# Kernel optimization log

Measured on AMD Instinct MI355X. Metric: run time of the kernel, lower is better.

## Reference

```python
import jax, jax.numpy as jnp
import numpy as np

NUM_SIN = 8
HIDDEN = 64
COND = 128
OUT = 4
SQRT2 = 1.4142135623730951


def coords_to_sinusoidals(coords):
    # coords: [..., 2]; per-frequency blocks of 4: [sin_x, sin_y, cos_x, cos_y]
    freqs = 2.0 ** jnp.arange(NUM_SIN, dtype=coords.dtype)  # mult freq_type, multiplier=2
    ang = coords[..., None, :] * freqs[:, None]              # [..., 8, 2]
    emb = jnp.concatenate([jnp.sin(ang), jnp.cos(ang)], axis=-1)  # [..., 8, 4]
    return emb.reshape(coords.shape[:-1] + (2 * 2 * NUM_SIN,))


def equal_linear(x, w, b, lrelu):
    scale = 1.0 / np.sqrt(w.shape[1])  # lr_mul = 1
    y = x @ (w * scale).T + b
    if lrelu:
        y = jax.nn.leaky_relu(y, 0.2) * SQRT2  # fused_lrelu
    return y


def setup_inputs() -> dict:
    key = jax.random.key(0)
    ks = jax.random.split(key, 8)
    coords = jax.random.normal(ks[0], (8, 256, 256, 2), dtype=jnp.float32)
    c = jax.random.normal(ks[1], (8, COND), dtype=jnp.float32)
    freq_unlock = jax.random.uniform(ks[2], (1,), dtype=jnp.float32)
    in1 = 2 * 2 * NUM_SIN + COND  # 160
    in2 = HIDDEN + COND           # 192
    w1 = jax.random.normal(ks[3], (HIDDEN, in1), dtype=jnp.float32)
    w2 = jax.random.normal(ks[4], (HIDDEN, in2), dtype=jnp.float32)
    w3 = jax.random.normal(ks[5], (HIDDEN, in2), dtype=jnp.float32)
    w4 = jax.random.normal(ks[6], (OUT, in2), dtype=jnp.float32)
    b1 = jnp.zeros((HIDDEN,), jnp.float32)
    b2 = jnp.zeros((HIDDEN,), jnp.float32)
    b3 = jnp.zeros((HIDDEN,), jnp.float32)
    b4 = jnp.zeros((OUT,), jnp.float32)
    return {"coords": coords, "c": c, "freq_unlock": freq_unlock,
            "w1": w1, "b1": b1, "w2": w2, "b2": b2,
            "w3": w3, "b3": b3, "w4": w4, "b4": b4}


def reference(coords, c, freq_unlock, w1, b1, w2, b2, w3, b3, w4, b4):
    B, H, W, _ = coords.shape
    emb = coords_to_sinusoidals(coords / 10.0)  # [B,H,W,32]
    # progressive frequency masking
    limits = jnp.arange(1, NUM_SIN + 1, dtype=coords.dtype) / (NUM_SIN + 1)
    weights = jnp.clip((freq_unlock[0] - limits) * (NUM_SIN + 1), 0.0, 1.0)  # [8]
    emb = emb * jnp.repeat(weights, 4)  # blocks of 4 per frequency
    x = emb.reshape(B * H * W, -1)
    cf = jnp.broadcast_to(c[:, None, None, :], (B, H, W, COND)).reshape(B * H * W, COND)
    h = equal_linear(jnp.concatenate([x, cf], -1), w1, b1, True)
    h = equal_linear(jnp.concatenate([h, cf], -1), w2, b2, True)
    h = equal_linear(jnp.concatenate([h, cf], -1), w3, b3, True)
    h = equal_linear(jnp.concatenate([h, cf], -1), w4, b4, False)
    out = h.reshape(B, H, W, OUT)
    # radius masking
    radius = jnp.sqrt(jnp.sum(coords ** 2, axis=-1, keepdims=True))
    out = out * (1.0 - jnp.tanh(jax.nn.relu(radius - 1.0)))
    return out
```

## Files before the change

kernel.cpp:

```cpp
#include <hip/hip_runtime.h>
#include <math.h>


typedef _Float16 half2v __attribute__((ext_vector_type(2)));
typedef __fp16   fp16x2 __attribute__((ext_vector_type(2)));
typedef _Float16 half4v __attribute__((ext_vector_type(4)));
typedef _Float16 half8  __attribute__((ext_vector_type(8)));
typedef float f32x16 __attribute__((ext_vector_type(16)));

#define SCALE1 0.0790569415042094833f
#define SCALE2 0.0721687836487032206f
#define SQRT2F 1.41421356237309515f

#define FE_L1 0
#define FE_L2 256
#define FE_L3 768
#define FE_L4 1280
#define FE_TOT 1536
#define OFF_CB1 6144
#define OFF_CB2 6656
#define OFF_CB3 7168
#define OFF_CB4 7680

__global__ __launch_bounds__(256) void prep_kernel(
    const float* __restrict__ c, const float* __restrict__ fu,
    const float* __restrict__ w1, const float* __restrict__ b1,
    const float* __restrict__ w2, const float* __restrict__ b2,
    const float* __restrict__ w3, const float* __restrict__ b3,
    const float* __restrict__ w4, const float* __restrict__ b4,
    float* __restrict__ ws)
{
  int t = blockIdx.x * 256 + threadIdx.x;
  if (t < 12288) {
    _Float16* fr = (_Float16*)ws;
    int e, Ktm;
    const float* w; float scale; int stride; bool perm;
    if (t < 2048)       { e = t;         Ktm = 2; w = w1; scale = SCALE1;          stride = 160; perm = false; }
    else if (t < 6144)  { e = t - 2048;  Ktm = 4; w = w2; scale = SCALE2 * SQRT2F; stride = 192; perm = true;  }
    else if (t < 10240) { e = t - 6144;  Ktm = 4; w = w3; scale = SCALE2 * SQRT2F; stride = 192; perm = true;  }
    else                { e = t - 10240; Ktm = 4; w = w4; scale = SCALE2 * SQRT2F; stride = 192; perm = true;  }
    int til  = e >> 9;
    int lane = (e >> 3) & 63;
    int r    = e & 7;
    int q    = lane >> 5;
    int mt = til / Ktm, kt = til - mt * Ktm;
    int j = 32 * mt + (lane & 31);
    int k;
    if (perm) {
      k = 32 * (kt >> 1) + 16 * (kt & 1) + 8 * (r >> 2) + 4 * q + (r & 3);
    } else {
      k = 16 * kt + 8 * q + r;
    }
    float val;
    if (t < 2048) {
      float mw = (fu[0] - (float)((k >> 2) + 1) * (1.0f / 9.0f)) * 9.0f;
      mw = fminf(fmaxf(mw, 0.0f), 1.0f);
      val = w[j * stride + k] * scale * mw;
    } else if (t >= 10240) {
      val = (j < 4) ? w[j * stride + k] * scale : 0.0f;
    } else {
      val = w[j * stride + k] * scale;
    }
    fr[t] = (_Float16)val;
  } else {
    int u = t - 12288;
    if (u >= 6272) return;
    int d = u >> 2, part = u & 3;
    const float* wr; float bias; float scale; int outoff;
    int b, j;
    if (d < 1536) {
      int grp = d >> 9;
      b = (d & 511) >> 6; j = d & 63;
      if (grp == 0)      { wr = w1 + j * 160 + 32; bias = b1[j]; scale = SCALE1; outoff = OFF_CB1 + b * 64 + j; }
      else if (grp == 1) { wr = w2 + j * 192 + 64; bias = b2[j]; scale = SCALE2; outoff = OFF_CB2 + b * 64 + j; }
      else               { wr = w3 + j * 192 + 64; bias = b3[j]; scale = SCALE2; outoff = OFF_CB3 + b * 64 + j; }
    } else {
      int u2 = d - 1536;
      b = u2 >> 2; j = u2 & 3;
      wr = w4 + j * 192 + 64; bias = b4[j]; scale = SCALE2; outoff = OFF_CB4 + b * 4 + j;
    }
    const float4* wv = (const float4*)wr + part * 8;
    const float4* cv = (const float4*)(c + b * 128) + part * 8;
    float4 s = make_float4(0.f, 0.f, 0.f, 0.f);
    #pragma unroll
    for (int k = 0; k < 8; ++k) {
      float4 a = wv[k], dd = cv[k];
      s.x = fmaf(a.x, dd.x, s.x);
      s.y = fmaf(a.y, dd.y, s.y);
      s.z = fmaf(a.z, dd.z, s.z);
      s.w = fmaf(a.w, dd.w, s.w);
    }
    float v = (s.x + s.y) + (s.z + s.w);
    v += __shfl_xor(v, 1);
    v += __shfl_xor(v, 2);
    if (part == 0) ws[outoff] = fmaf(scale, v, bias);
  }
}

#define WAIT_VM3() asm volatile("s_waitcnt vmcnt(3)" ::: "memory")
#define WAIT_VM0() asm volatile("s_waitcnt vmcnt(0)" ::: "memory")

__global__ __launch_bounds__(256, 4) void decoder_main(
    const float2* __restrict__ coords, const float* __restrict__ ws,
    float4* __restrict__ out)
{
  __shared__ __align__(16) _Float16 sfr_raw[FE_TOT * 8];
  __shared__ __align__(16) float scb[256];
  half8* __restrict__ sfr = (half8*)sfr_raw;

  const int tid  = threadIdx.x;
  const int lane = tid & 63;
  const int wave = tid >> 6;
  const int b    = blockIdx.x >> 7;
  const int col  = lane & 31;
  const bool hi  = lane >= 32;
  const int q4   = hi ? 4 : 0;

  const float2* __restrict__ cptr = coords + blockIdx.x * 512 + wave * 64;
  float2 cc[2][2];
  cc[0][0] = cptr[col];       cc[0][1] = cptr[32 + col];
  cc[1][0] = cptr[256 + col]; cc[1][1] = cptr[288 + col];
  __builtin_amdgcn_sched_barrier(0);

  if (wave == 3) {
    __builtin_amdgcn_global_load_lds(
        (const __attribute__((address_space(1))) void*)(ws + OFF_CB1 + b * 64 + lane),
        (__attribute__((address_space(3))) void*)(scb + 0), 4, 0, 0);
    __builtin_amdgcn_global_load_lds(
        (const __attribute__((address_space(1))) void*)(ws + OFF_CB2 + b * 64 + lane),
        (__attribute__((address_space(3))) void*)(scb + 64), 4, 0, 0);
    __builtin_amdgcn_global_load_lds(
        (const __attribute__((address_space(1))) void*)(ws + OFF_CB3 + b * 64 + lane),
        (__attribute__((address_space(3))) void*)(scb + 128), 4, 0, 0);
    __builtin_amdgcn_global_load_lds(
        (const __attribute__((address_space(1))) void*)(ws + OFF_CB4 + b * 4 + lane),
        (__attribute__((address_space(3))) void*)(scb + 192), 4, 0, 0);
  }
  __builtin_amdgcn_sched_barrier(0);

  const half8* __restrict__ gfr = (const half8*)ws;
  #pragma unroll
  for (int i = 0; i < 3; ++i) {
    const int e0 = wave * 64 + 256 * i;
    __builtin_amdgcn_global_load_lds(
        (const __attribute__((address_space(1))) void*)(gfr + e0 + lane),
        (__attribute__((address_space(3))) void*)(sfr_raw + e0 * 8),
        16, 0, 0);
  }
  __builtin_amdgcn_sched_barrier(0);
  #pragma unroll
  for (int i = 3; i < 6; ++i) {
    const int e0 = wave * 64 + 256 * i;
    __builtin_amdgcn_global_load_lds(
        (const __attribute__((address_space(1))) void*)(gfr + e0 + lane),
        (__attribute__((address_space(3))) void*)(sfr_raw + e0 * 8),
        16, 0, 0);
  }
  __builtin_amdgcn_sched_barrier(0);

  f32x16 acc[2][2];
  half8 nbf[2][4];

  auto transition = [&]() {
    #pragma unroll
    for (int mt = 0; mt < 2; ++mt)
      #pragma unroll
      for (int nt = 0; nt < 2; ++nt) {
        #pragma unroll
        for (int h = 0; h < 2; ++h) {
          half2v pp[4];
          #pragma unroll
          for (int p = 0; p < 4; ++p) {
            fp16x2 t = __builtin_amdgcn_cvt_pkrtz(acc[mt][nt][8 * h + 2 * p],
                                                  acc[mt][nt][8 * h + 2 * p + 1]);
            pp[p] = __builtin_bit_cast(half2v, t);
          }
          half4v q0 = __builtin_shufflevector(pp[0], pp[1], 0, 1, 2, 3);
          half4v q1 = __builtin_shufflevector(pp[2], pp[3], 0, 1, 2, 3);
          half8 f = __builtin_shufflevector(q0, q1, 0, 1, 2, 3, 4, 5, 6, 7);
          half8 f2 = f * (_Float16)0.2f;
          nbf[nt][2 * mt + h] = __builtin_elementwise_max(f, f2);
        }
      }
  };

  auto init_acc = [&](const float* __restrict__ cb) {
    #pragma unroll
    for (int mt = 0; mt < 2; ++mt)
      #pragma unroll
      for (int g = 0; g < 4; ++g) {
        const float4 f = *(const float4*)(cb + 32 * mt + 8 * g + q4);
        #pragma unroll
        for (int nt = 0; nt < 2; ++nt) {
          acc[mt][nt][4 * g + 0] = f.x;
          acc[mt][nt][4 * g + 1] = f.y;
          acc[mt][nt][4 * g + 2] = f.z;
          acc[mt][nt][4 * g + 3] = f.w;
        }
      }
  };

  #pragma unroll
  for (int t = 0; t < 2; ++t) {
    half8 bf[2][2];
    {
      const float qm = hi ? 0.4f : 0.1f;
      auto chain = [](float a, float* s, float* c) {
        float s0 = __sinf(a), c0 = __cosf(a);
        s[0] = s0; c[0] = c0;
        float s1 = 2.f * s0 * c0, c1 = (c0 - s0) * (c0 + s0);
        s[1] = s1; c[1] = c1;
        float s2 = 2.f * s1 * c1, c2 = (c1 - s1) * (c1 + s1);
        float s3 = 2.f * s2 * c2, c3 = (c2 - s2) * (c2 + s2);
        float s4 = 2.f * s3 * c3, c4 = (c3 - s3) * (c3 + s3);
        s[2] = s4; c[2] = c4;
        float s5 = 2.f * s4 * c4, c5 = (c4 - s4) * (c4 + s4);
        s[3] = s5; c[3] = c5;
      };
      #pragma unroll
      for (int nt = 0; nt < 2; ++nt) {
        const float2 ccv = cc[t][nt];
        float sx[4], cx[4], sy[4], cy[4];
        chain(ccv.x * qm, sx, cx);
        chain(ccv.y * qm, sy, cy);
        #pragma unroll
        for (int kt = 0; kt < 2; ++kt) {
          const int i0 = 2 * kt, i1 = 2 * kt + 1;
          half2v p0v = __builtin_bit_cast(half2v, __builtin_amdgcn_cvt_pkrtz(sx[i0], sy[i0]));
          half2v p1v = __builtin_bit_cast(half2v, __builtin_amdgcn_cvt_pkrtz(cx[i0], cy[i0]));
          half2v p2v = __builtin_bit_cast(half2v, __builtin_amdgcn_cvt_pkrtz(sx[i1], sy[i1]));
          half2v p3v = __builtin_bit_cast(half2v, __builtin_amdgcn_cvt_pkrtz(cx[i1], cy[i1]));
          half4v q0 = __builtin_shufflevector(p0v, p1v, 0, 1, 2, 3);
          half4v q1 = __builtin_shufflevector(p2v, p3v, 0, 1, 2, 3);
          bf[nt][kt] = __builtin_shufflevector(q0, q1, 0, 1, 2, 3, 4, 5, 6, 7);
        }
      }
    }

    if (t == 0) {
      WAIT_VM3();
      __builtin_amdgcn_s_barrier();
      __builtin_amdgcn_sched_barrier(0);
    }

    init_acc(scb + 0);
    #pragma unroll
    for (int kt = 0; kt < 2; ++kt) {
      half8 a0 = sfr[FE_L1 + (0 * 2 + kt) * 64 + lane];
      half8 a1 = sfr[FE_L1 + (1 * 2 + kt) * 64 + lane];
      acc[0][0] = __builtin_amdgcn_mfma_f32_32x32x16_f16(a0, bf[0][kt], acc[0][0], 0, 0, 0);
      acc[0][1] = __builtin_amdgcn_mfma_f32_32x32x16_f16(a0, bf[1][kt], acc[0][1], 0, 0, 0);
      acc[1][0] = __builtin_amdgcn_mfma_f32_32x32x16_f16(a1, bf[0][kt], acc[1][0], 0, 0, 0);
      acc[1][1] = __builtin_amdgcn_mfma_f32_32x32x16_f16(a1, bf[1][kt], acc[1][1], 0, 0, 0);
    }
    transition();

    init_acc(scb + 64);
    #pragma unroll
    for (int kt = 0; kt < 4; ++kt) {
      half8 a0 = sfr[FE_L2 + (0 * 4 + kt) * 64 + lane];
      half8 a1 = sfr[FE_L2 + (1 * 4 + kt) * 64 + lane];
      acc[0][0] = __builtin_amdgcn_mfma_f32_32x32x16_f16(a0, nbf[0][kt], acc[0][0], 0, 0, 0);
      acc[0][1] = __builtin_amdgcn_mfma_f32_32x32x16_f16(a0, nbf[1][kt], acc[0][1], 0, 0, 0);
      acc[1][0] = __builtin_amdgcn_mfma_f32_32x32x16_f16(a1, nbf[0][kt], acc[1][0], 0, 0, 0);
      acc[1][1] = __builtin_amdgcn_mfma_f32_32x32x16_f16(a1, nbf[1][kt], acc[1][1], 0, 0, 0);
    }
    transition();

    if (t == 0) {
      WAIT_VM0();
      __builtin_amdgcn_s_barrier();
      __builtin_amdgcn_sched_barrier(0);
    }

    init_acc(scb + 128);
    #pragma unroll
    for (int kt = 0; kt < 4; ++kt) {
      half8 a0 = sfr[FE_L3 + (0 * 4 + kt) * 64 + lane];
      half8 a1 = sfr[FE_L3 + (1 * 4 + kt) * 64 + lane];
      acc[0][0] = __builtin_amdgcn_mfma_f32_32x32x16_f16(a0, nbf[0][kt], acc[0][0], 0, 0, 0);
      acc[0][1] = __builtin_amdgcn_mfma_f32_32x32x16_f16(a0, nbf[1][kt], acc[0][1], 0, 0, 0);
      acc[1][0] = __builtin_amdgcn_mfma_f32_32x32x16_f16(a1, nbf[0][kt], acc[1][0], 0, 0, 0);
      acc[1][1] = __builtin_amdgcn_mfma_f32_32x32x16_f16(a1, nbf[1][kt], acc[1][1], 0, 0, 0);
    }
    transition();

    f32x16 acc4[2];
    {
      const float c0 = scb[192], c1 = scb[193], c2 = scb[194], c3 = scb[195];
      #pragma unroll
      for (int r = 0; r < 16; ++r) { acc4[0][r] = 0.f; acc4[1][r] = 0.f; }
      if (!hi) {
        acc4[0][0] = c0; acc4[0][1] = c1; acc4[0][2] = c2; acc4[0][3] = c3;
        acc4[1][0] = c0; acc4[1][1] = c1; acc4[1][2] = c2; acc4[1][3] = c3;
      }
    }
    #pragma unroll
    for (int kt = 0; kt < 4; ++kt) {
      half8 a0 = sfr[FE_L4 + kt * 64 + lane];
      acc4[0] = __builtin_amdgcn_mfma_f32_32x32x16_f16(a0, nbf[0][kt], acc4[0], 0, 0, 0);
      acc4[1] = __builtin_amdgcn_mfma_f32_32x32x16_f16(a0, nbf[1][kt], acc4[1], 0, 0, 0);
    }

    if (!hi) {
      const int pbase = blockIdx.x * 512 + t * 256 + wave * 64 + col;
      #pragma unroll
      for (int nt = 0; nt < 2; ++nt) {
        const float2 ccv = cc[t][nt];
        const float rad = sqrtf(ccv.x * ccv.x + ccv.y * ccv.y);
        const float tt = fmaxf(rad - 1.0f, 0.0f);
        const float m = 2.0f / (__expf(2.0f * tt) + 1.0f);
        out[pbase + 32 * nt] = make_float4(acc4[nt][0] * m, acc4[nt][1] * m,
                                           acc4[nt][2] * m, acc4[nt][3] * m);
      }
    }
  }
}

extern "C" void kernel_launch(void* const* d_in, const int* in_sizes, int n_in,
                              void* d_out, int out_size, void* d_ws, size_t ws_size,
                              hipStream_t stream) {
  const float* coords = (const float*)d_in[0];
  const float* c      = (const float*)d_in[1];
  const float* fu     = (const float*)d_in[2];
  const float* w1     = (const float*)d_in[3];
  const float* b1     = (const float*)d_in[4];
  const float* w2     = (const float*)d_in[5];
  const float* b2     = (const float*)d_in[6];
  const float* w3     = (const float*)d_in[7];
  const float* b3     = (const float*)d_in[8];
  const float* w4     = (const float*)d_in[9];
  const float* b4     = (const float*)d_in[10];
  float* ws  = (float*)d_ws;
  float* out = (float*)d_out;

  int npix = in_sizes[0] / 2;

  prep_kernel<<<73, 256, 0, stream>>>(c, fu, w1, b1, w2, b2, w3, b3, w4, b4, ws);
  decoder_main<<<npix / 512, 256, 0, stream>>>(
      (const float2*)coords, ws, (float4*)out);
}
```

Measured before the change: 92.70 us.

## Initialize accumulators via bias MFMA with split-fp16 bias fragments

The per-image conditioning bias is now written by the prep kernel as fp16 hi/lo pairs laid out as MFMA A-fragments, alongside the weights. The main kernel loads them into LDS with the weight fragments and produces each layer's initial accumulator with an MFMA against a ones vector, instead of filling 16-wide accumulators from LDS float4 reads and register moves. The radius mask computation is hoisted earlier so it overlaps other work. This trades VALU/LDS accumulator initialization for extra MFMA issues and a larger LDS footprint, which could lower occupancy.

```diff
diff --git a/kernel.cpp b/kernel.cpp
--- a/kernel.cpp
+++ b/kernel.cpp
@@ -17,10 +17,8 @@
 #define FE_L3 768
 #define FE_L4 1280
 #define FE_TOT 1536
-#define OFF_CB1 6144
-#define OFF_CB2 6656
-#define OFF_CB3 7168
-#define OFF_CB4 7680
+#define BE_BASE 1536
+#define BIAS_PER_IMG 512
 
 __global__ __launch_bounds__(256) void prep_kernel(
     const float* __restrict__ c, const float* __restrict__ fu,
@@ -62,22 +60,23 @@
       val = w[j * stride + k] * scale;
     }
     fr[t] = (_Float16)val;
-  } else {
+  } else if (t < 18560) {
     int u = t - 12288;
-    if (u >= 6272) return;
     int d = u >> 2, part = u & 3;
-    const float* wr; float bias; float scale; int outoff;
-    int b, j;
+    const float* wr; float bias; float scale;
+    int b, j, entry, lidx;
     if (d < 1536) {
       int grp = d >> 9;
       b = (d & 511) >> 6; j = d & 63;
-      if (grp == 0)      { wr = w1 + j * 160 + 32; bias = b1[j]; scale = SCALE1; outoff = OFF_CB1 + b * 64 + j; }
-      else if (grp == 1) { wr = w2 + j * 192 + 64; bias = b2[j]; scale = SCALE2; outoff = OFF_CB2 + b * 64 + j; }
-      else               { wr = w3 + j * 192 + 64; bias = b3[j]; scale = SCALE2; outoff = OFF_CB3 + b * 64 + j; }
+      if (grp == 0)      { wr = w1 + j * 160 + 32; bias = b1[j]; scale = SCALE1; }
+      else if (grp == 1) { wr = w2 + j * 192 + 64; bias = b2[j]; scale = SCALE2; }
+      else               { wr = w3 + j * 192 + 64; bias = b3[j]; scale = SCALE2; }
+      entry = grp * 2 + (j >> 5); lidx = j & 31;
     } else {
       int u2 = d - 1536;
       b = u2 >> 2; j = u2 & 3;
-      wr = w4 + j * 192 + 64; bias = b4[j]; scale = SCALE2; outoff = OFF_CB4 + b * 4 + j;
+      wr = w4 + j * 192 + 64; bias = b4[j]; scale = SCALE2;
+      entry = 6; lidx = j;
     }
     const float4* wv = (const float4*)wr + part * 8;
     const float4* cv = (const float4*)(c + b * 128) + part * 8;
@@ -93,7 +92,24 @@
     float v = (s.x + s.y) + (s.z + s.w);
     v += __shfl_xor(v, 1);
     v += __shfl_xor(v, 2);
-    if (part == 0) ws[outoff] = fmaf(scale, v, bias);
+    if (part == 0) {
+      float vf = fmaf(scale, v, bias);
+      _Float16 hi16 = (_Float16)vf;
+      _Float16 lo16 = (_Float16)(vf - (float)hi16);
+      half8 o = {};
+      o[0] = hi16; o[1] = lo16;
+      ((half8*)ws)[BE_BASE + b * BIAS_PER_IMG + entry * 64 + lidx] = o;
+    }
+  } else {
+    int u = t - 18560;
+    if (u >= 2528) return;
+    int img = u / 316, rem = u - img * 316;
+    int entry, lidx;
+    if (rem < 224)      { entry = rem >> 5; lidx = 32 + (rem & 31); }
+    else if (rem < 252) { entry = 6;        lidx = 4 + (rem - 224); }
+    else                { entry = 7;        lidx = rem - 252; }
+    half8 z8 = {};
+    ((half8*)ws)[BE_BASE + img * BIAS_PER_IMG + entry * 64 + lidx] = z8;
   }
 }
 
@@ -104,8 +120,7 @@
     const float2* __restrict__ coords, const float* __restrict__ ws,
     float4* __restrict__ out)
 {
-  __shared__ __align__(16) _Float16 sfr_raw[FE_TOT * 8];
-  __shared__ __align__(16) float scb[256];
+  __shared__ __align__(16) _Float16 sfr_raw[(FE_TOT + BIAS_PER_IMG) * 8];
   half8* __restrict__ sfr = (half8*)sfr_raw;
 
   const int tid  = threadIdx.x;
@@ -114,7 +129,6 @@
   const int b    = blockIdx.x >> 7;
   const int col  = lane & 31;
   const bool hi  = lane >= 32;
-  const int q4   = hi ? 4 : 0;
 
   const float2* __restrict__ cptr = coords + blockIdx.x * 512 + wave * 64;
   float2 cc[2][2];
@@ -122,23 +136,16 @@
   cc[1][0] = cptr[256 + col]; cc[1][1] = cptr[288 + col];
   __builtin_amdgcn_sched_barrier(0);
 
-  if (wave == 3) {
+  const half8* __restrict__ gfr = (const half8*)ws;
+  #pragma unroll
+  for (int e = 0; e < 2; ++e) {
+    const int eL = BE_BASE + wave * 128 + 64 * e;
     __builtin_amdgcn_global_load_lds(
-        (const __attribute__((address_space(1))) void*)(ws + OFF_CB1 + b * 64 + lane),
-        (__attribute__((address_space(3))) void*)(scb + 0), 4, 0, 0);
-    __builtin_amdgcn_global_load_lds(
-        (const __attribute__((address_space(1))) void*)(ws + OFF_CB2 + b * 64 + lane),
-        (__attribute__((address_space(3))) void*)(scb + 64), 4, 0, 0);
-    __builtin_amdgcn_global_load_lds(
-        (const __attribute__((address_space(1))) void*)(ws + OFF_CB3 + b * 64 + lane),
-        (__attribute__((address_space(3))) void*)(scb + 128), 4, 0, 0);
-    __builtin_amdgcn_global_load_lds(
-        (const __attribute__((address_space(1))) void*)(ws + OFF_CB4 + b * 4 + lane),
-        (__attribute__((address_space(3))) void*)(scb + 192), 4, 0, 0);
+        (const __attribute__((address_space(1))) void*)(gfr + b * BIAS_PER_IMG + eL + lane),
+        (__attribute__((address_space(3))) void*)(sfr_raw + eL * 8),
+        16, 0, 0);
   }
   __builtin_amdgcn_sched_barrier(0);
-
-  const half8* __restrict__ gfr = (const half8*)ws;
   #pragma unroll
   for (int i = 0; i < 3; ++i) {
     const int e0 = wave * 64 + 256 * i;
@@ -157,6 +164,10 @@
         16, 0, 0);
   }
   __builtin_amdgcn_sched_barrier(0);
+
+  half8 bones = {};
+  if (!hi) { bones[0] = (_Float16)1.0f; bones[1] = (_Float16)1.0f; }
+  const f32x16 z = {};
 
   f32x16 acc[2][2];
   half8 nbf[2][4];
@@ -184,25 +195,10 @@
       }
   };
 
-  auto init_acc = [&](const float* __restrict__ cb) {
-    #pragma unroll
-    for (int mt = 0; mt < 2; ++mt)
-      #pragma unroll
-      for (int g = 0; g < 4; ++g) {
-        const float4 f = *(const float4*)(cb + 32 * mt + 8 * g + q4);
-        #pragma unroll
-        for (int nt = 0; nt < 2; ++nt) {
-          acc[mt][nt][4 * g + 0] = f.x;
-          acc[mt][nt][4 * g + 1] = f.y;
-          acc[mt][nt][4 * g + 2] = f.z;
-          acc[mt][nt][4 * g + 3] = f.w;
-        }
-      }
-  };
-
   #pragma unroll
   for (int t = 0; t < 2; ++t) {
     half8 bf[2][2];
+    float mm[2];
     {
       const float qm = hi ? 0.4f : 0.1f;
       auto chain = [](float a, float* s, float* c) {
@@ -220,6 +216,9 @@
       #pragma unroll
       for (int nt = 0; nt < 2; ++nt) {
         const float2 ccv = cc[t][nt];
+        const float rad = sqrtf(ccv.x * ccv.x + ccv.y * ccv.y);
+        const float tt = fmaxf(rad - 1.0f, 0.0f);
+        mm[nt] = 2.0f / (__expf(2.0f * tt) + 1.0f);
         float sx[4], cx[4], sy[4], cy[4];
         chain(ccv.x * qm, sx, cx);
         chain(ccv.y * qm, sy, cy);
@@ -243,7 +242,14 @@
       __builtin_amdgcn_sched_barrier(0);
     }
 
-    init_acc(scb + 0);
+    {
+      half8 ba0 = sfr[BE_BASE + 0 * 64 + lane];
+      half8 ba1 = sfr[BE_BASE + 1 * 64 + lane];
+      acc[0][0] = __builtin_amdgcn_mfma_f32_32x32x16_f16(ba0, bones, z, 0, 0, 0);
+      acc[0][1] = __builtin_amdgcn_mfma_f32_32x32x16_f16(ba0, bones, z, 0, 0, 0);
+      acc[1][0] = __builtin_amdgcn_mfma_f32_32x32x16_f16(ba1, bones, z, 0, 0, 0);
+      acc[1][1] = __builtin_amdgcn_mfma_f32_32x32x16_f16(ba1, bones, z, 0, 0, 0);
+    }
     #pragma unroll
     for (int kt = 0; kt < 2; ++kt) {
       half8 a0 = sfr[FE_L1 + (0 * 2 + kt) * 64 + lane];
@@ -255,7 +261,14 @@
     }
     transition();
 
-    init_acc(scb + 64);
+    {
+      half8 ba0 = sfr[BE_BASE + 2 * 64 + lane];
+      half8 ba1 = sfr[BE_BASE + 3 * 64 + lane];
+      acc[0][0] = __builtin_amdgcn_mfma_f32_32x32x16_f16(ba0, bones, z, 0, 0, 0);
+      acc[0][1] = __builtin_amdgcn_mfma_f32_32x32x16_f16(ba0, bones, z, 0, 0, 0);
+      acc[1][0] = __builtin_amdgcn_mfma_f32_32x32x16_f16(ba1, bones, z, 0, 0, 0);
+      acc[1][1] = __builtin_amdgcn_mfma_f32_32x32x16_f16(ba1, bones, z, 0, 0, 0);
+    }
     #pragma unroll
     for (int kt = 0; kt < 4; ++kt) {
       half8 a0 = sfr[FE_L2 + (0 * 4 + kt) * 64 + lane];
@@ -273,7 +286,14 @@
       __builtin_amdgcn_sched_barrier(0);
     }
 
-    init_acc(scb + 128);
+    {
+      half8 ba0 = sfr[BE_BASE + 4 * 64 + lane];
+      half8 ba1 = sfr[BE_BASE + 5 * 64 + lane];
+      acc[0][0] = __builtin_amdgcn_mfma_f32_32x32x16_f16(ba0, bones, z, 0, 0, 0);
+      acc[0][1] = __builtin_amdgcn_mfma_f32_32x32x16_f16(ba0, bones, z, 0, 0, 0);
+      acc[1][0] = __builtin_amdgcn_mfma_f32_32x32x16_f16(ba1, bones, z, 0, 0, 0);
+      acc[1][1] = __builtin_amdgcn_mfma_f32_32x32x16_f16(ba1, bones, z, 0, 0, 0);
+    }
     #pragma unroll
     for (int kt = 0; kt < 4; ++kt) {
       half8 a0 = sfr[FE_L3 + (0 * 4 + kt) * 64 + lane];
@@ -287,13 +307,9 @@
 
     f32x16 acc4[2];
     {
-      const float c0 = scb[192], c1 = scb[193], c2 = scb[194], c3 = scb[195];
-      #pragma unroll
-      for (int r = 0; r < 16; ++r) { acc4[0][r] = 0.f; acc4[1][r] = 0.f; }
-      if (!hi) {
-        acc4[0][0] = c0; acc4[0][1] = c1; acc4[0][2] = c2; acc4[0][3] = c3;
-        acc4[1][0] = c0; acc4[1][1] = c1; acc4[1][2] = c2; acc4[1][3] = c3;
-      }
+      half8 ba = sfr[BE_BASE + 6 * 64 + lane];
+      acc4[0] = __builtin_amdgcn_mfma_f32_32x32x16_f16(ba, bones, z, 0, 0, 0);
+      acc4[1] = __builtin_amdgcn_mfma_f32_32x32x16_f16(ba, bones, z, 0, 0, 0);
     }
     #pragma unroll
     for (int kt = 0; kt < 4; ++kt) {
@@ -306,10 +322,7 @@
       const int pbase = blockIdx.x * 512 + t * 256 + wave * 64 + col;
       #pragma unroll
       for (int nt = 0; nt < 2; ++nt) {
-        const float2 ccv = cc[t][nt];
-        const float rad = sqrtf(ccv.x * ccv.x + ccv.y * ccv.y);
-        const float tt = fmaxf(rad - 1.0f, 0.0f);
-        const float m = 2.0f / (__expf(2.0f * tt) + 1.0f);
+        const float m = mm[nt];
         out[pbase + 32 * nt] = make_float4(acc4[nt][0] * m, acc4[nt][1] * m,
                                            acc4[nt][2] * m, acc4[nt][3] * m);
       }
@@ -336,7 +349,7 @@
 
   int npix = in_sizes[0] / 2;
 
-  prep_kernel<<<73, 256, 0, stream>>>(c, fu, w1, b1, w2, b2, w3, b3, w4, b4, ws);
+  prep_kernel<<<83, 256, 0, stream>>>(c, fu, w1, b1, w2, b2, w3, b3, w4, b4, ws);
   decoder_main<<<npix / 512, 256, 0, stream>>>(
       (const float2*)coords, ws, (float4*)out);
 }
```

Result: slower. 96.88 us (+4.5%).
